# Performance work log

Hardware: AMD Instinct MI355X
Metric: run time of the kernel (lower is better)

## Reference

```python
import jax, jax.numpy as jnp
import numpy as np

NUM_USERS = 100000
NUM_ITEMS = 50000
NUM_HIDDEN = 64
NUM_BINS = 10
BATCH = 131072
N_QUAD = 64  # quadrature nodes in incomplete/complete beta
EPS = 1e-6


def _trapz0(y, dt):
    # trapezoidal rule along axis 0 with uniform spacing dt
    return (jnp.sum(y, axis=0) - 0.5 * (y[0] + y[-1])) * dt


def setup_inputs() -> dict:
    key = jax.random.key(0)
    ks = jax.random.split(key, 12)
    return {
        "uid_input": jax.random.randint(ks[0], (BATCH,), 0, NUM_USERS),
        "iid_input": jax.random.randint(ks[1], (BATCH,), 0, NUM_ITEMS),
        "uid_features": 0.1 * jax.random.normal(ks[2], (NUM_USERS, NUM_HIDDEN + 1), jnp.float32),
        "iid_features": 0.1 * jax.random.normal(ks[3], (NUM_ITEMS, NUM_HIDDEN + 1), jnp.float32),
        "uid_bin_terms": 0.1 * jax.random.normal(ks[4], (NUM_USERS, NUM_BINS), jnp.float32),
        "iid_bin_terms": 0.1 * jax.random.normal(ks[5], (NUM_ITEMS, NUM_BINS), jnp.float32),
        "uid_alpha_emb": 0.01 * jax.random.normal(ks[6], (NUM_USERS, 1), jnp.float32),
        "uid_beta_emb": 0.01 * jax.random.normal(ks[7], (NUM_USERS, 1), jnp.float32),
        "iid_alpha_emb": 0.01 * jax.random.normal(ks[8], (NUM_ITEMS, 1), jnp.float32),
        "iid_beta_emb": 0.01 * jax.random.normal(ks[9], (NUM_ITEMS, 1), jnp.float32),
        "global_bias": jnp.asarray(2.0, jnp.float32),
    }


def reference(uid_input, iid_input, uid_features, iid_features,
              uid_bin_terms, iid_bin_terms, uid_alpha_emb, uid_beta_emb,
              iid_alpha_emb, iid_beta_emb, global_bias):
    # embedding lookups (confidence features alias the regular features)
    uf = uid_features[uid_input]          # (B, H+1)
    vf = iid_features[iid_input]          # (B, H+1)
    u = uf[:, :-1]                        # (B, H)
    v = vf[:, :-1]

    # mu / upsilon (upsilon_layer_id == 2: |dot|)
    dot = jnp.sum(u * v, axis=-1, keepdims=True)                    # (B, 1)
    len_prod = (jnp.linalg.norm(u, axis=1, keepdims=True)
                * jnp.linalg.norm(v, axis=1, keepdims=True))
    mu = jnp.clip(0.5 + 0.5 * dot / jnp.maximum(len_prod, EPS), EPS, 1.0 - EPS)
    upsilon = jnp.maximum(jnp.abs(dot), EPS)

    # alpha / beta
    alpha = jnp.maximum(0.01, mu * upsilon)
    beta = jnp.maximum(0.01, upsilon - alpha)
    alpha = global_bias + alpha
    beta = global_bias + beta
    alpha = jnp.maximum(0.01, alpha + uid_alpha_emb[uid_input] + iid_alpha_emb[iid_input])  # (B,1)
    beta = jnp.maximum(0.01, beta + uid_beta_emb[uid_input] + iid_beta_emb[iid_input])      # (B,1)

    # per-pair bin edges via normalized exp + cumsum
    terms = jnp.exp(uid_bin_terms[uid_input] + iid_bin_terms[iid_input])  # (B, NUM_BINS)
    terms = terms / jnp.sum(terms, axis=-1, keepdims=True)
    edges = jnp.cumsum(terms, axis=-1)                                    # (B, NUM_BINS)

    # regularized incomplete beta at interior edges via trapezoidal quadrature
    x = edges[:, :-1]                                  # (B, NB-1)
    t = jnp.linspace(0.0, 1.0, N_QUAD, dtype=alpha.dtype)
    dt = t[1] - t[0]
    t3 = t[:, None, None]                              # (n, 1, 1)
    a3 = alpha[None, :, :]                             # (1, B, 1)
    b3 = beta[None, :, :]
    tx = t3 * x[None]                                  # (n, B, NB-1)
    integrand = (tx ** (a3 - 1.0)) * ((1.0 - tx) ** (b3 - 1.0))
    integrand = integrand * (t3 <= x[None]).astype(integrand.dtype)
    Bx_ab = _trapz0(integrand, dt)                     # (B, NB-1)

    # complete beta B(a, b)
    c_int = (t[None, :] ** (alpha - 1.0)) * ((1.0 - t[None, :]) ** (beta - 1.0))  # (B, n)
    B_ab = (jnp.sum(c_int, axis=-1) - 0.5 * (c_int[:, 0] + c_int[:, -1])) * dt    # (B,)

    cdf = Bx_ab / B_ab[:, None]                        # (B, NB-1)
    cdf = jnp.concatenate([cdf, jnp.ones_like(alpha)], axis=-1)  # (B, NB)
    mass = jnp.concatenate([cdf[:, :1], cdf[:, 1:] - cdf[:, :-1]], axis=-1)
    return mass
```

## Files before the change

kernel.cpp:

```cpp
#include <hip/hip_runtime.h>
#include <math.h>

#define BLOCK 256

__device__ __forceinline__ float exp2_fast(float x) {
#if __has_builtin(__builtin_amdgcn_exp2f)
    return __builtin_amdgcn_exp2f(x);
#else
    return __expf(x * 0.69314718055994531f);
#endif
}

__device__ __forceinline__ double exp_f64_fast(double x) {
    const double L2E = 1.4426950408889634074;
    const double LN2 = 0.69314718055994530942;
    double z = x * L2E;
    double n = rint(z);
    double r = fma(x, L2E, -n);
    double w = r * LN2;
    double p = 2.08767569878680989792e-9;
    p = fma(p, w, 2.50521083854417187751e-8);
    p = fma(p, w, 2.75573192239858906526e-7);
    p = fma(p, w, 2.75573192239858925110e-6);
    p = fma(p, w, 2.48015873015873015873e-5);
    p = fma(p, w, 1.98412698412698412698e-4);
    p = fma(p, w, 1.38888888888888888889e-3);
    p = fma(p, w, 8.33333333333333333333e-3);
    p = fma(p, w, 4.16666666666666666667e-2);
    p = fma(p, w, 1.66666666666666666667e-1);
    p = fma(p, w, 0.5);
    p = fma(p, w, 1.0);
    p = fma(p, w, 1.0);
    const int ni = (int)n;
    const double sc = __longlong_as_double((long long)(1023 + ni) << 52);
    return p * sc;
}

__global__ __launch_bounds__(BLOCK) void lbd_kernel(
    const int* __restrict__ uid_in, const int* __restrict__ iid_in,
    const float* __restrict__ uf,  const float* __restrict__ vf,
    const float* __restrict__ ubt, const float* __restrict__ ibt,
    const float* __restrict__ uae, const float* __restrict__ ube,
    const float* __restrict__ iae, const float* __restrict__ ibe,
    const float* __restrict__ gbp, float* __restrict__ out, int B)
{
    __shared__ float4 s_tab[64];
    const int tid = threadIdx.x;
    if (tid < 64) {
        const double STEP0 = 1.0 / 63.0;
        float tf = (float)((double)tid * STEP0);
        if (tid == 63) tf = 1.0f;
        s_tab[tid] = make_float4(tf, __log2f(tf), __log2f(1.0f - tf), 0.0f);
    }
    __syncthreads();

    const int sub = tid & 15;
    const int s0  = blockIdx.x * (BLOCK / 16) + (tid >> 4);
    const bool valid = (s0 < B);
    const int s = valid ? s0 : (B - 1);

    const int u = uid_in[s];
    const int v = iid_in[s];

    const long long ub = (long long)u * 65;
    const long long vb = (long long)v * 65;
    float fu0 = uf[ub + sub],      fv0 = vf[vb + sub];
    float fu1 = uf[ub + 16 + sub], fv1 = vf[vb + 16 + sub];
    float fu2 = uf[ub + 32 + sub], fv2 = vf[vb + 32 + sub];
    float fu3 = uf[ub + 48 + sub], fv3 = vf[vb + 48 + sub];

    float dotp = fu0 * fv0 + fu1 * fv1 + fu2 * fv2 + fu3 * fv3;
    float sup  = fu0 * fu0 + fu1 * fu1 + fu2 * fu2 + fu3 * fu3;
    float svp  = fv0 * fv0 + fv1 * fv1 + fv2 * fv2 + fv3 * fv3;
#pragma unroll
    for (int d = 1; d < 16; d <<= 1) {
        dotp += __shfl_xor(dotp, d, 64);
        sup  += __shfl_xor(sup,  d, 64);
        svp  += __shfl_xor(svp,  d, 64);
    }

    const float gb = gbp[0];
    const float len_prod = sqrtf(sup) * sqrtf(svp);
    const float EPS = 1e-6f;
    const float HI  = (float)(1.0 - 1e-6);
    float mu = 0.5f + (0.5f * dotp) / fmaxf(len_prod, EPS);
    mu = fminf(fmaxf(mu, EPS), HI);
    const float ups = fmaxf(fabsf(dotp), EPS);
    const float al0 = fmaxf(0.01f, mu * ups);
    const float be0 = fmaxf(0.01f, ups - al0);
    const float alpha = fmaxf(0.01f, (gb + al0) + uae[u] + iae[v]);
    const float beta  = fmaxf(0.01f, (gb + be0) + ube[u] + ibe[v]);
    const float am1 = alpha - 1.0f;
    const float bm1 = beta  - 1.0f;

    const double STEP = 1.0 / 63.0;
    float xf_own = 0.f, lx_own = 0.f;
    int   im_own = 0;
    {
        double e = 0.0;
        if (sub < 10)
            e = exp_f64_fast((double)ubt[u * 10 + sub] + (double)ibt[v * 10 + sub]);
        double c = e;
#pragma unroll
        for (int d = 1; d < 16; d <<= 1) {
            double t = __shfl_up(c, d, 16);
            if (sub >= d) c += t;
        }
        const double ssum = __shfl(c, 9, 16);
        if (sub < 9) {
            const double x = c / ssum;
            int im = (int)(x * 63.0);
            if (im > 62) im = 62;
            while (im < 62 && (double)(im + 1) * STEP <= x) ++im;
            while (im >= 1 && (double)im * STEP > x) --im;
            im_own = im;
            xf_own = (float)x;
            lx_own = __log2f(xf_own);
        }
    }
    float xfj[9], alxj[9];
    int   imj[9], imw[9];
#pragma unroll
    for (int j = 0; j < 9; ++j) {
        xfj[j]  = __shfl(xf_own, j, 16);
        alxj[j] = am1 * __shfl(lx_own, j, 16);
        imj[j]  = __shfl(im_own, j, 16);
        int mm  = imj[j];
        mm = max(mm, __shfl_xor(mm, 16, 64));
        mm = max(mm, __shfl_xor(mm, 32, 64));
        imw[j] = __builtin_amdgcn_readfirstlane(mm);
    }

    float tfm[4], altm[4], l1m[4];
#pragma unroll
    for (int m = 0; m < 4; ++m) {
        float4 e = s_tab[m * 16 + sub];
        tfm[m]  = e.x;
        altm[m] = am1 * e.y;
        l1m[m]  = e.z;
    }

    float accD = 0.0f;
    float acc[9];
#pragma unroll
    for (int j = 0; j < 9; ++j) acc[j] = 0.0f;

#define EVAL_MJ(m, j)                                                              \
    do {                                                                           \
        const float w_ = fmaf(-tfm[m], xfj[j], 1.0f);                              \
        const float e_ = fmaf(bm1, __log2f(w_), altm[m] + alxj[j]);                \
        const float y_ = exp2_fast(e_);                                            \
        const int   i_ = (m) * 16 + sub;                                           \
        acc[j] += ((unsigned)(i_ - 1) < (unsigned)imj[j]) ? y_ : 0.0f;             \
    } while (0)

#pragma unroll
    for (int m = 0; m < 4; ++m)
        accD += exp2_fast(fmaf(bm1, l1m[m], altm[m]));

#pragma unroll
    for (int j = 0; j < 9; ++j) EVAL_MJ(0, j);

#pragma unroll
    for (int m = 1; m < 4; ++m) {
#pragma unroll
        for (int j = 0; j < 9; ++j) {
            if (imw[j] >= 16 * m) EVAL_MJ(m, j);
        }
    }
#undef EVAL_MJ

#pragma unroll
    for (int d = 1; d < 16; d <<= 1) {
        accD += __shfl_xor(accD, d, 64);
#pragma unroll
        for (int j = 0; j < 9; ++j) acc[j] += __shfl_xor(acc[j], d, 64);
    }

    const float dtf = (float)(1.0 / 63.0);
    const float Bab = accD * dtf;
    const float rB  = 1.0f / Bab;
    float cdfv[9];
#pragma unroll
    for (int j = 0; j < 9; ++j) cdfv[j] = (acc[j] * dtf) * rB;

    float mo = cdfv[0];
#pragma unroll
    for (int j = 1; j < 9; ++j) mo = (sub == j) ? (cdfv[j] - cdfv[j - 1]) : mo;
    mo = (sub == 9) ? (1.0f - cdfv[8]) : mo;
    if (valid && sub < 10) out[(long long)s * 10 + sub] = mo;
}

extern "C" void kernel_launch(void* const* d_in, const int* in_sizes, int n_in,
                              void* d_out, int out_size, void* d_ws, size_t ws_size,
                              hipStream_t stream) {
    (void)n_in; (void)out_size; (void)d_ws; (void)ws_size;
    const int*   uid = (const int*)d_in[0];
    const int*   iid = (const int*)d_in[1];
    const float* uf  = (const float*)d_in[2];
    const float* vf  = (const float*)d_in[3];
    const float* ubt = (const float*)d_in[4];
    const float* ibt = (const float*)d_in[5];
    const float* uae = (const float*)d_in[6];
    const float* ube = (const float*)d_in[7];
    const float* iae = (const float*)d_in[8];
    const float* ibe = (const float*)d_in[9];
    const float* gb  = (const float*)d_in[10];
    float* out = (float*)d_out;
    const int B = in_sizes[0];
    const int samples_per_block = BLOCK / 16;
    const int grid = (B + samples_per_block - 1) / samples_per_block;
    hipLaunchKernelGGL(lbd_kernel, dim3(grid), dim3(BLOCK), 0, stream,
                       uid, iid, uf, vf, ubt, ibt, uae, ube, iae, ibe, gb, out, B);
}
```

Baseline: 137.8 us.

## Drop shared quadrature table and wave skip; use 4-wide feature loads

Each lane now loads four contiguous feature floats through a 4-float struct instead of four strided scalars. The shared-memory table of quadrature nodes and their logs, along with its __syncthreads, is replaced by per-thread log2 computation. The wave-uniform check that skipped whole quadrature chunks beyond the largest edge is removed, so all 36 node/edge evaluations always run and are masked per lane. The bin-index correction loops become a branchless plus-or-minus one adjustment. This trades barrier, LDS and branch overhead for more transcendental work per lane, and the 4-float loads stay only 4-byte aligned because rows are 65 floats wide.

```diff
diff --git a/kernel.cpp b/kernel.cpp
--- a/kernel.cpp
+++ b/kernel.cpp
@@ -2,6 +2,8 @@
 #include <math.h>
 
 #define BLOCK 256
+
+struct F4a4 { float a, b, c, d; };
 
 __device__ __forceinline__ float exp2_fast(float x) {
 #if __has_builtin(__builtin_amdgcn_exp2f)
@@ -44,16 +46,7 @@
     const float* __restrict__ iae, const float* __restrict__ ibe,
     const float* __restrict__ gbp, float* __restrict__ out, int B)
 {
-    __shared__ float4 s_tab[64];
     const int tid = threadIdx.x;
-    if (tid < 64) {
-        const double STEP0 = 1.0 / 63.0;
-        float tf = (float)((double)tid * STEP0);
-        if (tid == 63) tf = 1.0f;
-        s_tab[tid] = make_float4(tf, __log2f(tf), __log2f(1.0f - tf), 0.0f);
-    }
-    __syncthreads();
-
     const int sub = tid & 15;
     const int s0  = blockIdx.x * (BLOCK / 16) + (tid >> 4);
     const bool valid = (s0 < B);
@@ -62,16 +55,12 @@
     const int u = uid_in[s];
     const int v = iid_in[s];
 
-    const long long ub = (long long)u * 65;
-    const long long vb = (long long)v * 65;
-    float fu0 = uf[ub + sub],      fv0 = vf[vb + sub];
-    float fu1 = uf[ub + 16 + sub], fv1 = vf[vb + 16 + sub];
-    float fu2 = uf[ub + 32 + sub], fv2 = vf[vb + 32 + sub];
-    float fu3 = uf[ub + 48 + sub], fv3 = vf[vb + 48 + sub];
+    const F4a4 a = ((const F4a4*)(uf + (long long)u * 65))[sub];
+    const F4a4 b = ((const F4a4*)(vf + (long long)v * 65))[sub];
 
-    float dotp = fu0 * fv0 + fu1 * fv1 + fu2 * fv2 + fu3 * fv3;
-    float sup  = fu0 * fu0 + fu1 * fu1 + fu2 * fu2 + fu3 * fu3;
-    float svp  = fv0 * fv0 + fv1 * fv1 + fv2 * fv2 + fv3 * fv3;
+    float dotp = a.a * b.a + a.b * b.b + a.c * b.c + a.d * b.d;
+    float sup  = a.a * a.a + a.b * a.b + a.c * a.c + a.d * a.d;
+    float svp  = b.a * b.a + b.b * b.b + b.c * b.c + b.d * b.d;
 #pragma unroll
     for (int d = 1; d < 16; d <<= 1) {
         dotp += __shfl_xor(dotp, d, 64);
@@ -109,35 +98,32 @@
         const double ssum = __shfl(c, 9, 16);
         if (sub < 9) {
             const double x = c / ssum;
-            int im = (int)(x * 63.0);
-            if (im > 62) im = 62;
-            while (im < 62 && (double)(im + 1) * STEP <= x) ++im;
-            while (im >= 1 && (double)im * STEP > x) --im;
-            im_own = im;
+            int k = (int)(x * 63.0);
+            k = (k > 62) ? 62 : k;
+            const int dec = ((double)k * STEP > x) ? 1 : 0;
+            const int inc = ((k < 62) && ((double)(k + 1) * STEP <= x)) ? 1 : 0;
+            im_own = k + inc - dec;
             xf_own = (float)x;
             lx_own = __log2f(xf_own);
         }
     }
     float xfj[9], alxj[9];
-    int   imj[9], imw[9];
+    int   imj[9];
 #pragma unroll
     for (int j = 0; j < 9; ++j) {
         xfj[j]  = __shfl(xf_own, j, 16);
         alxj[j] = am1 * __shfl(lx_own, j, 16);
         imj[j]  = __shfl(im_own, j, 16);
-        int mm  = imj[j];
-        mm = max(mm, __shfl_xor(mm, 16, 64));
-        mm = max(mm, __shfl_xor(mm, 32, 64));
-        imw[j] = __builtin_amdgcn_readfirstlane(mm);
     }
 
     float tfm[4], altm[4], l1m[4];
 #pragma unroll
     for (int m = 0; m < 4; ++m) {
-        float4 e = s_tab[m * 16 + sub];
-        tfm[m]  = e.x;
-        altm[m] = am1 * e.y;
-        l1m[m]  = e.z;
+        const int i = m * 16 + sub;
+        const float tf = (float)((double)i * STEP);
+        tfm[m]  = tf;
+        altm[m] = am1 * __log2f(tf);
+        l1m[m]  = __log2f(1.0f - tf);
     }
 
     float accD = 0.0f;
@@ -145,30 +131,21 @@
 #pragma unroll
     for (int j = 0; j < 9; ++j) acc[j] = 0.0f;
 
-#define EVAL_MJ(m, j)                                                              \
-    do {                                                                           \
-        const float w_ = fmaf(-tfm[m], xfj[j], 1.0f);                              \
-        const float e_ = fmaf(bm1, __log2f(w_), altm[m] + alxj[j]);                \
-        const float y_ = exp2_fast(e_);                                            \
-        const int   i_ = (m) * 16 + sub;                                           \
-        acc[j] += ((unsigned)(i_ - 1) < (unsigned)imj[j]) ? y_ : 0.0f;             \
-    } while (0)
-
 #pragma unroll
     for (int m = 0; m < 4; ++m)
         accD += exp2_fast(fmaf(bm1, l1m[m], altm[m]));
 
 #pragma unroll
-    for (int j = 0; j < 9; ++j) EVAL_MJ(0, j);
-
-#pragma unroll
-    for (int m = 1; m < 4; ++m) {
+    for (int m = 0; m < 4; ++m) {
 #pragma unroll
         for (int j = 0; j < 9; ++j) {
-            if (imw[j] >= 16 * m) EVAL_MJ(m, j);
+            const float w_ = fmaf(-tfm[m], xfj[j], 1.0f);
+            const float e_ = fmaf(bm1, __log2f(w_), altm[m] + alxj[j]);
+            const float y_ = exp2_fast(e_);
+            const int   i_ = m * 16 + sub;
+            acc[j] += ((unsigned)(i_ - 1) < (unsigned)imj[j]) ? y_ : 0.0f;
         }
     }
-#undef EVAL_MJ
 
 #pragma unroll
     for (int d = 1; d < 16; d <<= 1) {
```

After: 133.0 us. 1.04x faster.
